# Kernel optimization log

Measured on AMD Instinct MI355X. Metric: run time of the kernel, lower is better.

## Reference

```python
import jax, jax.numpy as jnp
import numpy as np
import math

B, S, E = 2, 4096, 2048
H, HKV, DK, DV = 16, 4, 128, 128
WIN = 512
EPS = 1e-5
NEG = -1e30


def setup_inputs() -> dict:
    key = jax.random.key(0)
    ks = jax.random.split(key, 8)
    scale = 1.0 / math.sqrt(E)
    return {
        "embeddings": jax.random.normal(ks[0], (B, S, E), dtype=jnp.float32),
        "cos_buffer": jax.random.uniform(ks[1], (2, 1, S, DK), dtype=jnp.float32),
        "sin_buffer": jax.random.uniform(ks[2], (2, 1, S, DK), dtype=jnp.float32),
        "wq": jax.random.normal(ks[3], (E, H * DK), dtype=jnp.float32) * scale,
        "wk": jax.random.normal(ks[4], (E, HKV * DK), dtype=jnp.float32) * scale,
        "wv": jax.random.normal(ks[5], (E, HKV * DV), dtype=jnp.float32) * scale,
        "wo": jax.random.normal(ks[6], (H * DV, E), dtype=jnp.float32) * (1.0 / math.sqrt(H * DV)),
        "window_size": WIN,
    }


def _rotate(f, cos, sin):
    half = f.shape[-1] // 2
    swapped = jnp.concatenate([f[..., half:], f[..., :half]], axis=-1)
    return cos * f + sin * swapped


def reference(embeddings, cos_buffer, sin_buffer, wq, wk, wv, wo, window_size):
    b, s, _ = embeddings.shape
    normed = embeddings * jax.lax.rsqrt(
        jnp.mean(jnp.square(embeddings), axis=-1, keepdims=True) + EPS)
    q = (normed @ wq).reshape(b, s, H, DK).transpose(0, 2, 1, 3)
    k = (normed @ wk).reshape(b, s, HKV, DK).transpose(0, 2, 1, 3)
    v = (normed @ wv).reshape(b, s, HKV, DV).transpose(0, 2, 1, 3)

    q = _rotate(q, cos_buffer[0], sin_buffer[0])
    k = _rotate(k, cos_buffer[1], sin_buffer[1])

    g = H // HKV
    k = jnp.repeat(k, g, axis=1)
    v = jnp.repeat(v, g, axis=1)

    W = window_size
    nb = s // W
    qb = q.reshape(b, H, nb, W, DK)
    kb = k.reshape(b, H, nb, W, DK)
    vb = v.reshape(b, H, nb, W, DV)
    k_prev = jnp.pad(kb, ((0, 0), (0, 0), (1, 0), (0, 0), (0, 0)))[:, :, :nb]
    v_prev = jnp.pad(vb, ((0, 0), (0, 0), (1, 0), (0, 0), (0, 0)))[:, :, :nb]
    kcat = jnp.concatenate([k_prev, kb], axis=3)
    vcat = jnp.concatenate([v_prev, vb], axis=3)

    scores = jnp.einsum('bhnqd,bhnkd->bhnqk', qb, kcat) / math.sqrt(DK)

    i = jnp.arange(W)[:, None]
    j = jnp.arange(2 * W)[None, :]
    base = (j > i) & (j <= i + W)
    blk = jnp.arange(nb)[:, None, None]
    mask = base[None] & ((blk > 0) | (j[None] >= W))
    scores = jnp.where(mask[None, None], scores, NEG)

    probs = jax.nn.softmax(scores, axis=-1)
    out = jnp.einsum('bhnqk,bhnkd->bhnqd', probs, vcat)
    out = out.reshape(b, H, s, DV).transpose(0, 2, 1, 3).reshape(b, s, H * DV)
    out = out @ wo
    return embeddings + out
```

## Files before the change

kernel.cpp:

```cpp
#include <hip/hip_runtime.h>

typedef unsigned short u16;
typedef __attribute__((ext_vector_type(8))) short s16x8;
typedef __attribute__((ext_vector_type(8))) unsigned short u16x8;
typedef __attribute__((ext_vector_type(4))) unsigned short u16x4;
typedef __attribute__((ext_vector_type(4))) float f32x4;

#define DEV __device__ __forceinline__

DEV u16 f2bf(float x) {
  union { float f; unsigned u; } c; c.f = x;
  unsigned r = c.u + 0x7FFFu + ((c.u >> 16) & 1u);
  return (u16)(r >> 16);
}
DEV float bf2f(u16 u) {
  union { unsigned u; float f; } c; c.u = ((unsigned)u) << 16;
  return c.f;
}
DEV void gload_lds16(const void* g, void* l) {
  __builtin_amdgcn_global_load_lds((const __attribute__((address_space(1))) void*)g,
                                   (__attribute__((address_space(3))) void*)l, 16, 0, 0);
}

__global__ __launch_bounds__(256) void k_rmsnorm(const float* __restrict__ emb, u16* __restrict__ X) {
  const int row = blockIdx.x;
  const int t = threadIdx.x;
  const float4* p4 = (const float4*)(emb + (size_t)row * 2048);
  float4 v0 = p4[t * 2], v1 = p4[t * 2 + 1];
  float ss = v0.x * v0.x + v0.y * v0.y + v0.z * v0.z + v0.w * v0.w
           + v1.x * v1.x + v1.y * v1.y + v1.z * v1.z + v1.w * v1.w;
  for (int off = 32; off; off >>= 1) ss += __shfl_xor(ss, off);
  __shared__ float red[4];
  if ((t & 63) == 0) red[t >> 6] = ss;
  __syncthreads();
  float tot = red[0] + red[1] + red[2] + red[3];
  float inv = rsqrtf(tot * (1.0f / 2048.0f) + 1e-5f);
  float v[8] = {v0.x, v0.y, v0.z, v0.w, v1.x, v1.y, v1.z, v1.w};
  u16x8 o;
  for (int j = 0; j < 8; ++j) o[j] = f2bf(v[j] * inv);
  *(u16x8*)(X + (size_t)row * 2048 + t * 8) = o;
}

__global__ __launch_bounds__(256) void k_transpose(const float* __restrict__ src, u16* __restrict__ dst,
                                                   int C, int dstStride) {
  __shared__ float tile[32][33];
  const int bc = blockIdx.x * 32, br = blockIdx.y * 32;
  const int tx = threadIdx.x & 31, ty = threadIdx.x >> 5;
  for (int i = 0; i < 32; i += 8)
    tile[ty + i][tx] = src[(size_t)(br + ty + i) * C + bc + tx];
  __syncthreads();
  for (int i = 0; i < 32; i += 8)
    dst[(size_t)(bc + ty + i) * dstStride + br + tx] = f2bf(tile[tx][ty + i]);
}

template <int EPI>
__global__ __launch_bounds__(512) void k_gemm256(const u16* __restrict__ A, const u16* __restrict__ Bt,
                                                 const int N, const int K, const int NBN,
                                                 u16* __restrict__ Cb, const float* __restrict__ Emb,
                                                 float* __restrict__ Cf,
                                                 u16* __restrict__ VtOut, const int vcol0) {
  __shared__ u16 Asm[2][256 * 64];
  __shared__ u16 Bsm[2][256 * 64];
  const int t = threadIdx.x, w = t >> 6, l = t & 63, g = (l >> 4), cc = l & 15;
  const int wm = w >> 2, wn = w & 3;

  const int lin = blockIdx.x;
  const int bm = lin / NBN, bn = lin % NBN;
  const size_t m0 = (size_t)bm * 256, n0 = (size_t)bn * 256;

  const int srow = t >> 3, sch = t & 7;

  auto stA = [&](int kt, int p, int pass) {
    const int row = pass * 64 + srow;
    const int c2 = sch ^ (row & 7);
    gload_lds16(A + (m0 + row) * K + kt * 64 + c2 * 8, &Asm[p][row * 64 + sch * 8]);
  };
  auto stB = [&](int kt, int p, int pass) {
    const int row = pass * 64 + srow;
    const int c2 = sch ^ (row & 7);
    gload_lds16(Bt + (n0 + row) * K + kt * 64 + c2 * 8, &Bsm[p][row * 64 + sch * 8]);
  };

  f32x4 acc[8][4];
#pragma unroll
  for (int mi = 0; mi < 8; ++mi)
#pragma unroll
    for (int ni = 0; ni < 4; ++ni) acc[mi][ni] = (f32x4){0.f, 0.f, 0.f, 0.f};

  const int NT = K >> 6;
#pragma unroll
  for (int pass = 0; pass < 4; ++pass) { stA(0, 0, pass); stB(0, 0, pass); }
  __syncthreads();

  for (int kt = 0; kt < NT; ++kt) {
    const int p = kt & 1;
    const bool pf = (kt + 1 < NT);
    const u16* Ap = &Asm[p][0];
    const u16* Bp = &Bsm[p][0];

    s16x8 bf[2][4];
#pragma unroll
    for (int kk = 0; kk < 2; ++kk)
#pragma unroll
      for (int ni = 0; ni < 4; ++ni) {
        const int row = wn * 64 + ni * 16 + cc;
        bf[kk][ni] = *(const s16x8*)&Bp[row * 64 + (((kk * 4 + g) ^ (row & 7)) * 8)];
      }

#pragma unroll
    for (int q = 0; q < 4; ++q) {
      s16x8 af[2][2];
#pragma unroll
      for (int kk = 0; kk < 2; ++kk)
#pragma unroll
        for (int m2 = 0; m2 < 2; ++m2) {
          const int row = wm * 128 + (q * 2 + m2) * 16 + cc;
          af[kk][m2] = *(const s16x8*)&Ap[row * 64 + (((kk * 4 + g) ^ (row & 7)) * 8)];
        }
      if (pf) {
        if (q == 0) { stA(kt + 1, p ^ 1, 0); stA(kt + 1, p ^ 1, 1); stB(kt + 1, p ^ 1, 0); }
        else if (q == 1) { stA(kt + 1, p ^ 1, 2); stA(kt + 1, p ^ 1, 3); stB(kt + 1, p ^ 1, 1); }
        else if (q == 2) { stB(kt + 1, p ^ 1, 2); stB(kt + 1, p ^ 1, 3); }
      }
#pragma unroll
      for (int m2 = 0; m2 < 2; ++m2)
#pragma unroll
        for (int ni = 0; ni < 4; ++ni)
#pragma unroll
          for (int kk = 0; kk < 2; ++kk)
            acc[q * 2 + m2][ni] =
                __builtin_amdgcn_mfma_f32_16x16x32_bf16(af[kk][m2], bf[kk][ni], acc[q * 2 + m2][ni], 0, 0, 0);
    }
    __syncthreads();
  }

  if (EPI == 1) {
#pragma unroll
    for (int mi = 0; mi < 8; ++mi)
#pragma unroll
      for (int ni = 0; ni < 4; ++ni)
#pragma unroll
        for (int r = 0; r < 4; ++r) {
          const size_t row = m0 + wm * 128 + mi * 16 + g * 4 + r;
          const size_t col = n0 + wn * 64 + ni * 16 + cc;
          Cf[row * N + col] = acc[mi][ni][r] + Emb[row * N + col];
        }
  } else if ((int)n0 >= vcol0) {
    const int bb = (int)(m0 >> 12);
    const int s0base = (int)(m0 & 4095);
#pragma unroll
    for (int mi = 0; mi < 8; ++mi)
#pragma unroll
      for (int ni = 0; ni < 4; ++ni) {
        const int dcol = (int)(n0 - vcol0) + wn * 64 + ni * 16 + cc;
        const int hkv = dcol >> 7, d = dcol & 127;
        const int s = s0base + wm * 128 + mi * 16 + g * 4;
        u16x4 o;
#pragma unroll
        for (int r = 0; r < 4; ++r) o[r] = f2bf(acc[mi][ni][r]);
        *(u16x4*)(VtOut + ((size_t)(bb * 4 + hkv) * 128 + d) * 4096 + s) = o;
      }
  } else {
#pragma unroll
    for (int mi = 0; mi < 8; ++mi)
#pragma unroll
      for (int ni = 0; ni < 4; ++ni)
#pragma unroll
        for (int r = 0; r < 4; ++r) {
          const size_t row = m0 + wm * 128 + mi * 16 + g * 4 + r;
          const size_t col = n0 + wn * 64 + ni * 16 + cc;
          Cb[row * N + col] = f2bf(acc[mi][ni][r]);
        }
  }
}

__global__ __launch_bounds__(192) void k_rope(const u16* __restrict__ qkv, const float* __restrict__ cosb,
                                              const float* __restrict__ sinb, u16* __restrict__ Q,
                                              u16* __restrict__ K) {
  const int row = blockIdx.x;
  const int b = row >> 12, s = row & 4095;
  const int t = threadIdx.x;
  const u16* src = qkv + (size_t)row * 3072;
  if (t < 128) {
    const int h = t >> 3, d0 = (t & 7) * 8;
    const float* cp = cosb + (size_t)s * 128;
    const float* sp = sinb + (size_t)s * 128;
    u16x8 lo = *(const u16x8*)(src + h * 128 + d0);
    u16x8 hi = *(const u16x8*)(src + h * 128 + d0 + 64);
    u16x8 olo, ohi;
    for (int j = 0; j < 8; ++j) {
      float fl = bf2f(lo[j]), fh = bf2f(hi[j]);
      olo[j] = f2bf(cp[d0 + j] * fl + sp[d0 + j] * fh);
      ohi[j] = f2bf(cp[d0 + 64 + j] * fh + sp[d0 + 64 + j] * fl);
    }
    u16* dq = Q + (((size_t)b * 16 + h) * 4096 + s) * 128;
    *(u16x8*)(dq + d0) = olo;
    *(u16x8*)(dq + d0 + 64) = ohi;
  } else if (t < 160) {
    const int idx = t - 128, hk = idx >> 3, d0 = (idx & 7) * 8;
    const float* cp = cosb + 524288 + (size_t)s * 128;
    const float* sp = sinb + 524288 + (size_t)s * 128;
    u16x8 lo = *(const u16x8*)(src + 2048 + hk * 128 + d0);
    u16x8 hi = *(const u16x8*)(src + 2048 + hk * 128 + d0 + 64);
    u16x8 olo, ohi;
    for (int j = 0; j < 8; ++j) {
      float fl = bf2f(lo[j]), fh = bf2f(hi[j]);
      olo[j] = f2bf(cp[d0 + j] * fl + sp[d0 + j] * fh);
      ohi[j] = f2bf(cp[d0 + 64 + j] * fh + sp[d0 + 64 + j] * fl);
    }
    u16* dk = K + (((size_t)b * 4 + hk) * 4096 + s) * 128;
    *(u16x8*)(dk + d0) = olo;
    *(u16x8*)(dk + d0 + 64) = ohi;
  }
}

__global__ __launch_bounds__(256) void k_attn(const u16* __restrict__ Q, const u16* __restrict__ K,
                                              const u16* __restrict__ Vt, u16* __restrict__ AO) {
  const int bid = blockIdx.x;
  const int lin = (bid & 7) * 128 + (bid >> 3);
  const int grp = lin >> 7;
  const int b = grp >> 2, hkv = grp & 3;
  const int rem = lin & 127;
  const int h = hkv * 4 + (rem >> 5);
  const int qt = rem & 31;

  const int t = threadIdx.x, w = t >> 6, l = t & 63, g = l >> 4, cc = l & 15;
  const int q0 = qt * 128;
  const int myq0 = q0 + w * 32;
  const u16* Qp = Q + (((size_t)b * 16 + h) * 4096 + q0) * 128;
  const u16* Kp = K + ((size_t)b * 4 + hkv) * 4096 * 128;
  const u16* Vp = Vt + ((size_t)b * 4 + hkv) * 128 * 4096;

  __shared__ u16 Kl[2][32 * 128];
  __shared__ u16 Vl[2][128 * 32];
  __shared__ u16 Ps[4][32 * 40];
  u16* myPs = &Ps[w][0];

  auto stage = [&](int kt, int bufi) {
    for (int pass = 0; pass < 2; ++pass) {
      const int m = pass * 256 + t;
      const int row = m >> 4, cst = m & 15;
      const int cor = cst ^ (row & 7);
      gload_lds16(Kp + (size_t)(kt * 32 + row) * 128 + cor * 8, &Kl[bufi][m * 8]);
    }
    for (int pass = 0; pass < 2; ++pass) {
      const int m = pass * 256 + t;
      const int d = m >> 2, cst = m & 3;
      const int cor = cst ^ (d & 3);
      gload_lds16(Vp + (size_t)d * 4096 + kt * 32 + cor * 8, &Vl[bufi][m * 8]);
    }
  };

  s16x8 qf[2][4];
  for (int mi = 0; mi < 2; ++mi)
    for (int kk = 0; kk < 4; ++kk)
      qf[mi][kk] = *(const s16x8*)(Qp + (size_t)(w * 32 + mi * 16 + cc) * 128 + kk * 32 + g * 8);

  f32x4 accO[2][8];
  for (int mi = 0; mi < 2; ++mi)
    for (int nd = 0; nd < 8; ++nd) accO[mi][nd] = (f32x4){0.f, 0.f, 0.f, 0.f};
  float mrun[2], lrun[2];
  for (int mi = 0; mi < 2; ++mi) { mrun[mi] = -1e30f; lrun[mi] = 0.f; }

  int lo = q0 - 511; if (lo < 0) lo = 0;
  const int kt_lo = lo >> 5, kt_hi = (q0 + 127) >> 5;
  const float scale = 0.08838834764831845f;

  int cur = 0;
  stage(kt_lo, 0);
  __syncthreads();

  for (int kt = kt_lo; kt <= kt_hi; ++kt) {
    if (kt < kt_hi) stage(kt + 1, cur ^ 1);

    const int k0 = kt * 32;
    const bool haswork = (k0 <= myq0 + 31) && (k0 + 31 >= myq0 - 511);
    const bool fullw   = (k0 + 31 <= myq0) && (k0 >= myq0 - 480);

    if (haswork) {
      f32x4 sc[2][2];
      for (int mi = 0; mi < 2; ++mi)
        for (int nk = 0; nk < 2; ++nk) sc[mi][nk] = (f32x4){0.f, 0.f, 0.f, 0.f};
      __builtin_amdgcn_s_setprio(1);
      for (int kk = 0; kk < 4; ++kk) {
        s16x8 kb[2];
        for (int nk = 0; nk < 2; ++nk) {
          const int row = nk * 16 + cc;
          kb[nk] = *(const s16x8*)&Kl[cur][row * 128 + (((kk * 4 + g) ^ (row & 7)) * 8)];
        }
        for (int mi = 0; mi < 2; ++mi)
          for (int nk = 0; nk < 2; ++nk)
            sc[mi][nk] = __builtin_amdgcn_mfma_f32_16x16x32_bf16(kb[nk], qf[mi][kk], sc[mi][nk], 0, 0, 0);
      }
      __builtin_amdgcn_s_setprio(0);

      for (int mi = 0; mi < 2; ++mi) {
        const int qpos = myq0 + mi * 16 + cc;
        if (fullw) {
          for (int nk = 0; nk < 2; ++nk)
            for (int r = 0; r < 4; ++r) sc[mi][nk][r] *= scale;
        } else {
          for (int nk = 0; nk < 2; ++nk)
            for (int r = 0; r < 4; ++r) {
              const int kpos = k0 + nk * 16 + g * 4 + r;
              const float v = sc[mi][nk][r] * scale;
              sc[mi][nk][r] = (kpos <= qpos && kpos + 512 > qpos) ? v : -1e30f;
            }
        }
        float rm = sc[mi][0][0];
        for (int nk = 0; nk < 2; ++nk)
          for (int r = 0; r < 4; ++r) rm = fmaxf(rm, sc[mi][nk][r]);
        rm = fmaxf(rm, __shfl_xor(rm, 16));
        rm = fmaxf(rm, __shfl_xor(rm, 32));
        const float mnew = fmaxf(mrun[mi], rm);
        float rs = 0.f;
        if (fullw) {
          for (int nk = 0; nk < 2; ++nk)
            for (int r = 0; r < 4; ++r) {
              float pv = __expf(sc[mi][nk][r] - mnew);
              sc[mi][nk][r] = pv;
              rs += pv;
            }
        } else {
          for (int nk = 0; nk < 2; ++nk)
            for (int r = 0; r < 4; ++r) {
              float pv = sc[mi][nk][r];
              pv = (pv <= -1e29f) ? 0.f : __expf(pv - mnew);
              sc[mi][nk][r] = pv;
              rs += pv;
            }
        }
        rs += __shfl_xor(rs, 16);
        rs += __shfl_xor(rs, 32);
        const float alpha = __expf(mrun[mi] - mnew);
        mrun[mi] = mnew;
        lrun[mi] = lrun[mi] * alpha + rs;
        for (int nd = 0; nd < 8; ++nd)
          for (int r = 0; r < 4; ++r) accO[mi][nd][r] *= alpha;
        for (int nk = 0; nk < 2; ++nk) {
          u16x4 o;
          for (int r = 0; r < 4; ++r) o[r] = f2bf(sc[mi][nk][r]);
          *(u16x4*)&myPs[(mi * 16 + cc) * 40 + nk * 16 + g * 4] = o;
        }
      }

      __builtin_amdgcn_s_setprio(1);
      {
        s16x8 pa[2];
        for (int mi = 0; mi < 2; ++mi)
          pa[mi] = *(const s16x8*)&myPs[(mi * 16 + cc) * 40 + g * 8];
        for (int nd = 0; nd < 8; ++nd) {
          const int d = nd * 16 + cc;
          s16x8 vb = *(const s16x8*)&Vl[cur][d * 32 + ((g ^ (d & 3)) * 8)];
          for (int mi = 0; mi < 2; ++mi)
            accO[mi][nd] = __builtin_amdgcn_mfma_f32_16x16x32_bf16(vb, pa[mi], accO[mi][nd], 0, 0, 0);
        }
      }
      __builtin_amdgcn_s_setprio(0);
    }

    __syncthreads();
    cur ^= 1;
  }

  u16* op = AO + ((size_t)b * 4096 + q0) * 2048 + (size_t)h * 128;
  for (int mi = 0; mi < 2; ++mi) {
    const float inv = 1.0f / lrun[mi];
    for (int nd = 0; nd < 8; ++nd) {
      u16x4 o;
      for (int r = 0; r < 4; ++r) o[r] = f2bf(accO[mi][nd][r] * inv);
      *(u16x4*)(op + (size_t)(w * 32 + mi * 16 + cc) * 2048 + nd * 16 + g * 4) = o;
    }
  }
}

extern "C" void kernel_launch(void* const* d_in, const int* in_sizes, int n_in,
                              void* d_out, int out_size, void* d_ws, size_t ws_size,
                              hipStream_t stream) {
  const float* emb  = (const float*)d_in[0];
  const float* cosb = (const float*)d_in[1];
  const float* sinb = (const float*)d_in[2];
  const float* wq   = (const float*)d_in[3];
  const float* wk   = (const float*)d_in[4];
  const float* wv   = (const float*)d_in[5];
  const float* wo   = (const float*)d_in[6];
  float* out = (float*)d_out;

  char* ws = (char*)d_ws;
  size_t off = 0;
  auto alloc = [&](size_t bytes) -> void* {
    void* p = ws + off;
    off += (bytes + 255) & ~(size_t)255;
    return p;
  };
  u16* X   = (u16*)alloc((size_t)8192 * 2048 * 2);
  u16* Wt  = (u16*)alloc((size_t)3072 * 2048 * 2);
  u16* Wot = (u16*)alloc((size_t)2048 * 2048 * 2);
  u16* qkv = (u16*)alloc((size_t)8192 * 3072 * 2);
  u16* Qb  = (u16*)alloc((size_t)2 * 16 * 4096 * 128 * 2);
  u16* Kb  = (u16*)alloc((size_t)2 * 4 * 4096 * 128 * 2);
  u16* VtB = (u16*)alloc((size_t)2 * 4 * 128 * 4096 * 2);
  u16* AOb = X;

  k_transpose<<<dim3(64, 64), 256, 0, stream>>>(wq, Wt, 2048, 2048);
  k_transpose<<<dim3(16, 64), 256, 0, stream>>>(wk, Wt + (size_t)2048 * 2048, 512, 2048);
  k_transpose<<<dim3(16, 64), 256, 0, stream>>>(wv, Wt + (size_t)2560 * 2048, 512, 2048);
  k_transpose<<<dim3(64, 64), 256, 0, stream>>>(wo, Wot, 2048, 2048);
  k_rmsnorm<<<8192, 256, 0, stream>>>(emb, X);
  k_gemm256<0><<<dim3(384), 512, 0, stream>>>(X, Wt, 3072, 2048, 12, qkv, nullptr, nullptr, VtB, 2560);
  k_rope<<<8192, 192, 0, stream>>>(qkv, cosb, sinb, Qb, Kb);
  k_attn<<<dim3(1024), 256, 0, stream>>>(Qb, Kb, VtB, AOb);
  k_gemm256<1><<<dim3(256), 512, 0, stream>>>(AOb, Wot, 2048, 2048, 8, nullptr, emb, out, nullptr, 1 << 30);
}
```

Before: 357.8 us.

## Fuse RoPE into QKV GEMM epilogue and drop intermediate qkv buffer

Remaps each wave's B-tile columns so a thread's four N-fragments hold matching low/high halves of each 128-wide head (d and d+64). This lets the QKV GEMM epilogue apply rotary embedding directly and write Q and K in head-major layout. The separate rope kernel and the 8192x3072 bf16 qkv buffer round trip go away. In exchange the epilogue does scattered 2-byte stores and per-element cos/sin loads, and the column remap also changes the output GEMM's indexing.

```diff
diff --git a/kernel.cpp b/kernel.cpp
--- a/kernel.cpp
+++ b/kernel.cpp
@@ -56,9 +56,10 @@
 template <int EPI>
 __global__ __launch_bounds__(512) void k_gemm256(const u16* __restrict__ A, const u16* __restrict__ Bt,
                                                  const int N, const int K, const int NBN,
-                                                 u16* __restrict__ Cb, const float* __restrict__ Emb,
-                                                 float* __restrict__ Cf,
-                                                 u16* __restrict__ VtOut, const int vcol0) {
+                                                 const float* __restrict__ cosb, const float* __restrict__ sinb,
+                                                 u16* __restrict__ Qb, u16* __restrict__ Kb,
+                                                 u16* __restrict__ VtOut,
+                                                 const float* __restrict__ Emb, float* __restrict__ Cf) {
   __shared__ u16 Asm[2][256 * 64];
   __shared__ u16 Bsm[2][256 * 64];
   const int t = threadIdx.x, w = t >> 6, l = t & 63, g = (l >> 4), cc = l & 15;
@@ -103,7 +104,7 @@
     for (int kk = 0; kk < 2; ++kk)
 #pragma unroll
       for (int ni = 0; ni < 4; ++ni) {
-        const int row = wn * 64 + ni * 16 + cc;
+        const int row = wn * 16 + ni * 64 + cc;
         bf[kk][ni] = *(const s16x8*)&Bp[row * 64 + (((kk * 4 + g) ^ (row & 7)) * 8)];
       }
 
@@ -142,17 +143,50 @@
 #pragma unroll
         for (int r = 0; r < 4; ++r) {
           const size_t row = m0 + wm * 128 + mi * 16 + g * 4 + r;
-          const size_t col = n0 + wn * 64 + ni * 16 + cc;
+          const size_t col = n0 + wn * 16 + ni * 64 + cc;
           Cf[row * N + col] = acc[mi][ni][r] + Emb[row * N + col];
         }
-  } else if ((int)n0 >= vcol0) {
+  } else if ((int)n0 < 2560) {
+    const bool isK = (int)n0 >= 2048;
+    const float* cbase = cosb + (isK ? 524288 : 0);
+    const float* sbase = sinb + (isK ? 524288 : 0);
+    const int dlo = wn * 16 + cc;
+#pragma unroll
+    for (int mi = 0; mi < 8; ++mi)
+#pragma unroll
+      for (int p = 0; p < 2; ++p) {
+        const int colbase = (int)n0 + p * 128;
+#pragma unroll
+        for (int r = 0; r < 4; ++r) {
+          const int row = (int)m0 + wm * 128 + mi * 16 + g * 4 + r;
+          const int bb = row >> 12, s = row & 4095;
+          const float lo = acc[mi][2 * p + 0][r];
+          const float hi = acc[mi][2 * p + 1][r];
+          const float* cpr = cbase + (size_t)s * 128;
+          const float* spr = sbase + (size_t)s * 128;
+          const u16 olo = f2bf(cpr[dlo] * lo + spr[dlo] * hi);
+          const u16 ohi = f2bf(cpr[dlo + 64] * hi + spr[dlo + 64] * lo);
+          if (!isK) {
+            const int h = colbase >> 7;
+            u16* dq = Qb + ((size_t)(bb * 16 + h) * 4096 + s) * 128;
+            dq[dlo] = olo;
+            dq[dlo + 64] = ohi;
+          } else {
+            const int hkv = (colbase - 2048) >> 7;
+            u16* dk = Kb + ((size_t)(bb * 4 + hkv) * 4096 + s) * 128;
+            dk[dlo] = olo;
+            dk[dlo + 64] = ohi;
+          }
+        }
+      }
+  } else {
     const int bb = (int)(m0 >> 12);
     const int s0base = (int)(m0 & 4095);
 #pragma unroll
     for (int mi = 0; mi < 8; ++mi)
 #pragma unroll
       for (int ni = 0; ni < 4; ++ni) {
-        const int dcol = (int)(n0 - vcol0) + wn * 64 + ni * 16 + cc;
+        const int dcol = (int)(n0 - 2560) + wn * 16 + ni * 64 + cc;
         const int hkv = dcol >> 7, d = dcol & 127;
         const int s = s0base + wm * 128 + mi * 16 + g * 4;
         u16x4 o;
@@ -160,57 +194,6 @@
         for (int r = 0; r < 4; ++r) o[r] = f2bf(acc[mi][ni][r]);
         *(u16x4*)(VtOut + ((size_t)(bb * 4 + hkv) * 128 + d) * 4096 + s) = o;
       }
-  } else {
-#pragma unroll
-    for (int mi = 0; mi < 8; ++mi)
-#pragma unroll
-      for (int ni = 0; ni < 4; ++ni)
-#pragma unroll
-        for (int r = 0; r < 4; ++r) {
-          const size_t row = m0 + wm * 128 + mi * 16 + g * 4 + r;
-          const size_t col = n0 + wn * 64 + ni * 16 + cc;
-          Cb[row * N + col] = f2bf(acc[mi][ni][r]);
-        }
-  }
-}
-
-__global__ __launch_bounds__(192) void k_rope(const u16* __restrict__ qkv, const float* __restrict__ cosb,
-                                              const float* __restrict__ sinb, u16* __restrict__ Q,
-                                              u16* __restrict__ K) {
-  const int row = blockIdx.x;
-  const int b = row >> 12, s = row & 4095;
-  const int t = threadIdx.x;
-  const u16* src = qkv + (size_t)row * 3072;
-  if (t < 128) {
-    const int h = t >> 3, d0 = (t & 7) * 8;
-    const float* cp = cosb + (size_t)s * 128;
-    const float* sp = sinb + (size_t)s * 128;
-    u16x8 lo = *(const u16x8*)(src + h * 128 + d0);
-    u16x8 hi = *(const u16x8*)(src + h * 128 + d0 + 64);
-    u16x8 olo, ohi;
-    for (int j = 0; j < 8; ++j) {
-      float fl = bf2f(lo[j]), fh = bf2f(hi[j]);
-      olo[j] = f2bf(cp[d0 + j] * fl + sp[d0 + j] * fh);
-      ohi[j] = f2bf(cp[d0 + 64 + j] * fh + sp[d0 + 64 + j] * fl);
-    }
-    u16* dq = Q + (((size_t)b * 16 + h) * 4096 + s) * 128;
-    *(u16x8*)(dq + d0) = olo;
-    *(u16x8*)(dq + d0 + 64) = ohi;
-  } else if (t < 160) {
-    const int idx = t - 128, hk = idx >> 3, d0 = (idx & 7) * 8;
-    const float* cp = cosb + 524288 + (size_t)s * 128;
-    const float* sp = sinb + 524288 + (size_t)s * 128;
-    u16x8 lo = *(const u16x8*)(src + 2048 + hk * 128 + d0);
-    u16x8 hi = *(const u16x8*)(src + 2048 + hk * 128 + d0 + 64);
-    u16x8 olo, ohi;
-    for (int j = 0; j < 8; ++j) {
-      float fl = bf2f(lo[j]), fh = bf2f(hi[j]);
-      olo[j] = f2bf(cp[d0 + j] * fl + sp[d0 + j] * fh);
-      ohi[j] = f2bf(cp[d0 + 64 + j] * fh + sp[d0 + 64 + j] * fl);
-    }
-    u16* dk = K + (((size_t)b * 4 + hk) * 4096 + s) * 128;
-    *(u16x8*)(dk + d0) = olo;
-    *(u16x8*)(dk + d0 + 64) = ohi;
   }
 }
 
@@ -396,7 +379,6 @@
   u16* X   = (u16*)alloc((size_t)8192 * 2048 * 2);
   u16* Wt  = (u16*)alloc((size_t)3072 * 2048 * 2);
   u16* Wot = (u16*)alloc((size_t)2048 * 2048 * 2);
-  u16* qkv = (u16*)alloc((size_t)8192 * 3072 * 2);
   u16* Qb  = (u16*)alloc((size_t)2 * 16 * 4096 * 128 * 2);
   u16* Kb  = (u16*)alloc((size_t)2 * 4 * 4096 * 128 * 2);
   u16* VtB = (u16*)alloc((size_t)2 * 4 * 128 * 4096 * 2);
@@ -407,8 +389,9 @@
   k_transpose<<<dim3(16, 64), 256, 0, stream>>>(wv, Wt + (size_t)2560 * 2048, 512, 2048);
   k_transpose<<<dim3(64, 64), 256, 0, stream>>>(wo, Wot, 2048, 2048);
   k_rmsnorm<<<8192, 256, 0, stream>>>(emb, X);
-  k_gemm256<0><<<dim3(384), 512, 0, stream>>>(X, Wt, 3072, 2048, 12, qkv, nullptr, nullptr, VtB, 2560);
-  k_rope<<<8192, 192, 0, stream>>>(qkv, cosb, sinb, Qb, Kb);
+  k_gemm256<0><<<dim3(384), 512, 0, stream>>>(X, Wt, 3072, 2048, 12, cosb, sinb, Qb, Kb, VtB,
+                                              nullptr, nullptr);
   k_attn<<<dim3(1024), 256, 0, stream>>>(Qb, Kb, VtB, AOb);
-  k_gemm256<1><<<dim3(256), 512, 0, stream>>>(AOb, Wot, 2048, 2048, 8, nullptr, emb, out, nullptr, 1 << 30);
-}
+  k_gemm256<1><<<dim3(256), 512, 0, stream>>>(AOb, Wot, 2048, 2048, 8, nullptr, nullptr, nullptr, nullptr,
+                                              nullptr, emb, out);
+}
```

New measurement: 338.2 us (median of 2 runs). 5.5% less time.
